# Performance work log

Measured on AMD Instinct MI355X. Metric: run time of the kernel, lower is better.

## Reference

```python
import jax, jax.numpy as jnp
import numpy as np

B, S, DX = 64, 4096, 512
Q, DQ = 128, 512

def setup_inputs() -> dict:
    key = jax.random.key(0)
    k1, k2, k3, k4 = jax.random.split(key, 4)
    x = jax.random.normal(k1, (B, S, DX), dtype=jnp.float32)
    query_matrix = jax.random.normal(k2, (B, Q, DQ), dtype=jnp.float32)
    # learned params (random_normal init in the original layer)
    W = jax.random.normal(k3, (DQ, DX), dtype=jnp.float32)
    p = jax.random.normal(k4, (Q, 1), dtype=jnp.float32)
    return {"x": x, "query_matrix": query_matrix, "W": W, "p": p}

def reference(x, query_matrix, W, p):
    # per-sample loop in the original: transpose(q_i) @ p -> [Dq, 1]; stacked & squeezed -> [B, Dq]
    new_q = jnp.einsum('bqd,q->bd', query_matrix, p[:, 0])          # [B, Dq]
    first = new_q @ W                                               # [B, Dx]
    scores = jnp.einsum('bd,bsd->bs', first, x)                     # [B, S]
    alpha = jax.nn.softmax(scores, axis=-1)                         # softmax over keys
    context = jnp.einsum('bs,bsd->bd', alpha, x)                    # batch_dot -> [B, Dx]
    return context
```

## Files before the change

### kernel.cpp

```cpp
#include <hip/hip_runtime.h>
#include <math.h>

#define BB 64
#define SS 4096
#define DXX 512
#define QQ 128
#define DQQ 512
#define SPLITS 32
#define CHUNK (SS / SPLITS)
#define NWAVES 4
#define ROWS_PER_WAVE (CHUNK / NWAVES)
#define RB 4

typedef float v4 __attribute__((ext_vector_type(4)));

__global__ __launch_bounds__(512) void compute_first(
        const float* __restrict__ qm, const float* __restrict__ W,
        const float* __restrict__ p, float* __restrict__ first) {
    int b = blockIdx.x;
    int t = threadIdx.x;
    __shared__ float sp[QQ];
    __shared__ float snq[DQQ];
    if (t < QQ) sp[t] = p[t];
    __syncthreads();

    const float* qb = qm + (size_t)b * QQ * DQQ + t;
    float acc = 0.f;
    #pragma unroll 8
    for (int q = 0; q < QQ; ++q) acc = fmaf(qb[(size_t)q * DQQ], sp[q], acc);
    snq[t] = acc;
    __syncthreads();

    float f = 0.f;
    #pragma unroll 8
    for (int dq = 0; dq < DQQ; ++dq) f = fmaf(snq[dq], W[(size_t)dq * DXX + t], f);
    first[b * DXX + t] = f;
}

__global__ __launch_bounds__(256) void attn_partial(
        const float* __restrict__ x, const float* __restrict__ first,
        float* __restrict__ pm, float* __restrict__ pl,
        float* __restrict__ pacc) {
    int blk  = blockIdx.x;
    int b    = blk / SPLITS;
    int sp   = blk % SPLITS;
    int tid  = threadIdx.x;
    int wave = tid >> 6;
    int lane = tid & 63;

    const float* fb = first + b * DXX;
    const v4 f0 = *(const v4*)(fb + lane * 4);
    const v4 f1 = *(const v4*)(fb + 256 + lane * 4);

    float m = -1e30f, l = 0.f;
    v4 a0 = {0.f, 0.f, 0.f, 0.f};
    v4 a1 = {0.f, 0.f, 0.f, 0.f};

    const float* xb = x + (size_t)b * SS * DXX;
    const int s0 = sp * CHUNK + wave;

    for (int i = 0; i < ROWS_PER_WAVE; i += RB) {
        v4 x0[RB], x1[RB];
        float d[RB];
        #pragma unroll
        for (int r = 0; r < RB; ++r) {
            const float* xr = xb + (size_t)(s0 + (i + r) * NWAVES) * DXX;
            x0[r] = __builtin_nontemporal_load((const v4*)(xr + lane * 4));
            x1[r] = __builtin_nontemporal_load((const v4*)(xr + 256 + lane * 4));
            v4 t4 = f0 * x0[r] + f1 * x1[r];
            d[r] = t4.x + t4.y + t4.z + t4.w;
        }
        #pragma unroll
        for (int off = 32; off > 0; off >>= 1) {
            #pragma unroll
            for (int r = 0; r < RB; ++r) d[r] += __shfl_xor(d[r], off, 64);
        }
        #pragma unroll
        for (int r = 0; r < RB; ++r) {
            if (d[r] > m) {
                const float alpha = __expf(m - d[r]);
                m = d[r];
                l = fmaf(l, alpha, 1.f);
                a0 = a0 * alpha + x0[r];
                a1 = a1 * alpha + x1[r];
            } else {
                const float w = __expf(d[r] - m);
                l += w;
                a0 += x0[r] * w;
                a1 += x1[r] * w;
            }
        }
    }

    __shared__ float sm[NWAVES];
    __shared__ float sl[NWAVES];
    __shared__ float sacc[NWAVES][DXX];
    if (lane == 0) { sm[wave] = m; sl[wave] = l; }
    float* sa = sacc[wave];
    *(v4*)(sa + lane * 4)       = a0;
    *(v4*)(sa + 256 + lane * 4) = a1;
    __syncthreads();

    const float M  = fmaxf(fmaxf(sm[0], sm[1]), fmaxf(sm[2], sm[3]));
    const float e0 = __expf(sm[0] - M), e1 = __expf(sm[1] - M);
    const float e2 = __expf(sm[2] - M), e3 = __expf(sm[3] - M);
    if (tid == 0) {
        pm[blk] = M;
        pl[blk] = sl[0] * e0 + sl[1] * e1 + sl[2] * e2 + sl[3] * e3;
    }
    #pragma unroll
    for (int dx = tid; dx < DXX; dx += 256) {
        pacc[(size_t)blk * DXX + dx] =
            sacc[0][dx] * e0 + sacc[1][dx] * e1 + sacc[2][dx] * e2 + sacc[3][dx] * e3;
    }
}

__global__ __launch_bounds__(256) void attn_finalize(
        const float* __restrict__ pm, const float* __restrict__ pl,
        const float* __restrict__ pacc, float* __restrict__ out) {
    int b = blockIdx.x;
    int tid = threadIdx.x;

    __shared__ float e[SPLITS];
    __shared__ float invL;
    if (tid == 0) {
        float M = -1e30f;
        for (int i = 0; i < SPLITS; ++i) M = fmaxf(M, pm[b * SPLITS + i]);
        float L = 0.f;
        for (int i = 0; i < SPLITS; ++i) {
            float ei = __expf(pm[b * SPLITS + i] - M);
            e[i] = ei;
            L += pl[b * SPLITS + i] * ei;
        }
        invL = 1.f / L;
    }
    __syncthreads();

    #pragma unroll
    for (int dx = tid; dx < DXX; dx += 256) {
        float v = 0.f;
        for (int i = 0; i < SPLITS; ++i)
            v = fmaf(pacc[(size_t)(b * SPLITS + i) * DXX + dx], e[i], v);
        out[b * DXX + dx] = v * invL;
    }
}

extern "C" void kernel_launch(void* const* d_in, const int* in_sizes, int n_in,
                              void* d_out, int out_size, void* d_ws, size_t ws_size,
                              hipStream_t stream) {
    const float* x  = (const float*)d_in[0];
    const float* qm = (const float*)d_in[1];
    const float* W  = (const float*)d_in[2];
    const float* p  = (const float*)d_in[3];
    float* out = (float*)d_out;

    float* ws    = (float*)d_ws;
    float* first = ws;
    float* pm    = first + BB * DXX;
    float* pl    = pm + BB * SPLITS;
    float* pacc  = pl + BB * SPLITS;

    compute_first<<<BB, 512, 0, stream>>>(qm, W, p, first);
    attn_partial<<<BB * SPLITS, 256, 0, stream>>>(x, first, pm, pl, pacc);
    attn_finalize<<<BB, 256, 0, stream>>>(pm, pl, pacc, out);
}
```

Measured before the change: 700.5 us.

## Double-buffer x row loads and use branchless online softmax in attention partial

```diff
diff --git a/kernel.cpp b/kernel.cpp
--- a/kernel.cpp
+++ b/kernel.cpp
@@ -11,6 +11,7 @@
 #define NWAVES 4
 #define ROWS_PER_WAVE (CHUNK / NWAVES)
 #define RB 4
+#define NGROUPS (ROWS_PER_WAVE / RB)
 
 typedef float v4 __attribute__((ext_vector_type(4)));
 
@@ -37,16 +38,16 @@
     first[b * DXX + t] = f;
 }
 
-__global__ __launch_bounds__(256) void attn_partial(
+__global__ __launch_bounds__(256, 4) void attn_partial(
         const float* __restrict__ x, const float* __restrict__ first,
         float* __restrict__ pm, float* __restrict__ pl,
         float* __restrict__ pacc) {
-    int blk  = blockIdx.x;
-    int b    = blk / SPLITS;
-    int sp   = blk % SPLITS;
-    int tid  = threadIdx.x;
-    int wave = tid >> 6;
-    int lane = tid & 63;
+    const int blk  = blockIdx.x;
+    const int b    = blk / SPLITS;
+    const int sp   = blk % SPLITS;
+    const int tid  = threadIdx.x;
+    const int wave = tid >> 6;
+    const int lane = tid & 63;
 
     const float* fb = first + b * DXX;
     const v4 f0 = *(const v4*)(fb + lane * 4);
@@ -56,41 +57,62 @@
     v4 a0 = {0.f, 0.f, 0.f, 0.f};
     v4 a1 = {0.f, 0.f, 0.f, 0.f};
 
-    const float* xb = x + (size_t)b * SS * DXX;
-    const int s0 = sp * CHUNK + wave;
+    const float* xw = x + (size_t)b * SS * DXX
+                        + (size_t)(sp * CHUNK + wave) * DXX + lane * 4;
+    const size_t rstep = (size_t)NWAVES * DXX;
 
-    for (int i = 0; i < ROWS_PER_WAVE; i += RB) {
-        v4 x0[RB], x1[RB];
-        float d[RB];
-        #pragma unroll
-        for (int r = 0; r < RB; ++r) {
-            const float* xr = xb + (size_t)(s0 + (i + r) * NWAVES) * DXX;
-            x0[r] = __builtin_nontemporal_load((const v4*)(xr + lane * 4));
-            x1[r] = __builtin_nontemporal_load((const v4*)(xr + 256 + lane * 4));
-            v4 t4 = f0 * x0[r] + f1 * x1[r];
-            d[r] = t4.x + t4.y + t4.z + t4.w;
-        }
-        #pragma unroll
-        for (int off = 32; off > 0; off >>= 1) {
-            #pragma unroll
-            for (int r = 0; r < RB; ++r) d[r] += __shfl_xor(d[r], off, 64);
-        }
-        #pragma unroll
-        for (int r = 0; r < RB; ++r) {
-            if (d[r] > m) {
-                const float alpha = __expf(m - d[r]);
-                m = d[r];
-                l = fmaf(l, alpha, 1.f);
-                a0 = a0 * alpha + x0[r];
-                a1 = a1 * alpha + x1[r];
-            } else {
-                const float w = __expf(d[r] - m);
-                l += w;
-                a0 += x0[r] * w;
-                a1 += x1[r] * w;
-            }
-        }
+    v4 pa0[RB], pa1[RB], pb0[RB], pb1[RB];
+
+#define LOADG(buf0, buf1, g)                                                 \
+    {                                                                        \
+        _Pragma("unroll")                                                    \
+        for (int r = 0; r < RB; ++r) {                                       \
+            const float* xr = xw + (size_t)((g) * RB + r) * rstep;           \
+            buf0[r] = *(const v4*)(xr);                                      \
+            buf1[r] = *(const v4*)(xr + 256);                                \
+        }                                                                    \
     }
+
+#define PROCESS(buf0, buf1)                                                  \
+    {                                                                        \
+        float d[RB];                                                         \
+        _Pragma("unroll")                                                    \
+        for (int r = 0; r < RB; ++r) {                                       \
+            v4 t4 = f0 * buf0[r] + f1 * buf1[r];                             \
+            d[r] = (t4.x + t4.y) + (t4.z + t4.w);                            \
+        }                                                                    \
+        _Pragma("unroll")                                                    \
+        for (int off = 32; off > 0; off >>= 1) {                             \
+            _Pragma("unroll")                                                \
+            for (int r = 0; r < RB; ++r) d[r] += __shfl_xor(d[r], off, 64);  \
+        }                                                                    \
+        _Pragma("unroll")                                                    \
+        for (int r = 0; r < RB; ++r) {                                       \
+            const float nm    = fmaxf(m, d[r]);                              \
+            const float alpha = __expf(m - nm);         \
+            const float w     = __expf(d[r] - nm);                           \
+            m = nm;                                                          \
+            l = fmaf(l, alpha, w);                                           \
+            a0 = a0 * alpha + buf0[r] * w;                                   \
+            a1 = a1 * alpha + buf1[r] * w;                                   \
+        }                                                                    \
+    }
+
+    LOADG(pa0, pa1, 0);
+
+    #pragma unroll
+    for (int g = 0; g < NGROUPS - 2; g += 2) {
+        LOADG(pb0, pb1, g + 1);
+        PROCESS(pa0, pa1);
+        LOADG(pa0, pa1, g + 2);
+        PROCESS(pb0, pb1);
+    }
+    LOADG(pb0, pb1, NGROUPS - 1);
+    PROCESS(pa0, pa1);
+    PROCESS(pb0, pb1);
+
+#undef LOADG
+#undef PROCESS
 
     __shared__ float sm[NWAVES];
     __shared__ float sl[NWAVES];
@@ -123,16 +145,18 @@
 
     __shared__ float e[SPLITS];
     __shared__ float invL;
-    if (tid == 0) {
-        float M = -1e30f;
-        for (int i = 0; i < SPLITS; ++i) M = fmaxf(M, pm[b * SPLITS + i]);
-        float L = 0.f;
-        for (int i = 0; i < SPLITS; ++i) {
-            float ei = __expf(pm[b * SPLITS + i] - M);
-            e[i] = ei;
-            L += pl[b * SPLITS + i] * ei;
-        }
-        invL = 1.f / L;
+    if (tid < 32) {
+        const float mv = pm[b * SPLITS + tid];
+        const float lv = pl[b * SPLITS + tid];
+        float M = mv;
+        #pragma unroll
+        for (int off = 16; off > 0; off >>= 1) M = fmaxf(M, __shfl_xor(M, off, 64));
+        const float ei = __expf(mv - M);
+        e[tid] = ei;
+        float L = lv * ei;
+        #pragma unroll
+        for (int off = 16; off > 0; off >>= 1) L += __shfl_xor(L, off, 64);
+        if (tid == 0) invL = 1.f / L;
     }
     __syncthreads();
 
```

After: 989.6 us. +41.3%, slower.
